# Performance work log

Measured on AMD Instinct MI355X. Metric: run time of the kernel, lower is better.

The kernel has to match this reference:

```python
import jax, jax.numpy as jnp
import numpy as np

NUM_HEADS = 12

def _get_rel_pos(size, rel_pos):
    # q_size == k_size == size, no interpolation needed (table has 2*size-1 rows)
    idx = jnp.arange(size)[:, None] - jnp.arange(size)[None, :] + (size - 1)  # (size,size)
    return rel_pos[idx]  # (size, size, head_dim)

def setup_inputs() -> dict:
    key = jax.random.key(0)
    ks = jax.random.split(key, 7)
    B, H, W, dim = 8, 32, 32, 768
    head_dim = dim // NUM_HEADS
    return {
        "x": jax.random.normal(ks[0], (B, H, W, dim), jnp.float32),
        "qkv_w": jax.random.normal(ks[1], (dim, 3 * dim), jnp.float32) * 0.02,
        "qkv_b": jax.random.normal(ks[2], (3 * dim,), jnp.float32) * 0.02,
        "proj_w": jax.random.normal(ks[3], (dim, dim), jnp.float32) * 0.02,
        "proj_b": jax.random.normal(ks[4], (dim,), jnp.float32) * 0.02,
        "rel_pos_h": jax.random.normal(ks[5], (2 * H - 1, head_dim), jnp.float32) * 0.02,
        "rel_pos_w": jax.random.normal(ks[6], (2 * W - 1, head_dim), jnp.float32) * 0.02,
    }

def reference(x, qkv_w, qkv_b, proj_w, proj_b, rel_pos_h, rel_pos_w):
    B, H, W, dim = x.shape
    N = H * W
    head_dim = dim // NUM_HEADS
    scale = head_dim ** (-0.5)

    qkv = x.reshape(B, N, dim) @ qkv_w + qkv_b                     # (B,N,3*dim)
    qkv = qkv.reshape(B, N, 3, NUM_HEADS, head_dim)
    qkv = qkv.transpose(2, 0, 3, 1, 4).reshape(3, B * NUM_HEADS, N, head_dim)
    q, k, v = qkv[0], qkv[1], qkv[2]                               # (B*h, N, hd)

    attn = jnp.einsum("bnd,bmd->bnm", q * scale, k)                # (B*h, N, N)

    # decomposed relative position bias
    Rh = _get_rel_pos(H, rel_pos_h)                                # (H,H,hd)
    Rw = _get_rel_pos(W, rel_pos_w)                                # (W,W,hd)
    r_q = q.reshape(B * NUM_HEADS, H, W, head_dim)
    rel_h = jnp.einsum("bhwc,hkc->bhwk", r_q, Rh)                  # (B*h,H,W,H)
    rel_w = jnp.einsum("bhwc,wkc->bhwk", r_q, Rw)                  # (B*h,H,W,W)
    attn = (attn.reshape(B * NUM_HEADS, H, W, H, W)
            + rel_h[:, :, :, :, None]
            + rel_w[:, :, :, None, :]).reshape(B * NUM_HEADS, N, N)

    attn = jax.nn.softmax(attn, axis=-1)
    out = jnp.einsum("bnm,bmd->bnd", attn, v)                      # (B*h, N, hd)
    out = out.reshape(B, NUM_HEADS, H, W, head_dim).transpose(0, 2, 3, 1, 4).reshape(B, H, W, dim)
    return out @ proj_w + proj_b
```

## Files before the change

### kernel.cpp

```cpp
#include <hip/hip_runtime.h>
#include <hip/hip_bf16.h>
#include <math.h>

#define DIM   768
#define NHEAD 12
#define NQ    1024

typedef short  short8  __attribute__((ext_vector_type(8)));
typedef unsigned short us8 __attribute__((ext_vector_type(8)));
typedef float  f32x16  __attribute__((ext_vector_type(16)));

#if __has_builtin(__builtin_amdgcn_exp2f)
#define EXP2(x) __builtin_amdgcn_exp2f(x)
#else
#define EXP2(x) __expf(0.69314718056f * (x))
#endif
#define LOG2E 1.44269504089f

__device__ inline ushort f2b(float f) {
  union { float f; unsigned u; } c; c.f = f;
  unsigned r = (c.u + 0x7FFFu + ((c.u >> 16) & 1u)) >> 16;
  return (ushort)r;
}
__device__ inline float b2f(ushort h) {
  union { unsigned u; float f; } c; c.u = ((unsigned)h) << 16;
  return c.f;
}
__device__ inline ushort4 cvt4(float4 v) {
  ushort4 o; o.x = f2b(v.x); o.y = f2b(v.y); o.z = f2b(v.z); o.w = f2b(v.w);
  return o;
}
__device__ inline unsigned pkr(float a, float b) {
  union { float f; unsigned u; } ca, cb; ca.f = a; cb.f = b;
  return __builtin_amdgcn_perm(cb.u + 0x8000u, ca.u + 0x8000u, 0x07060302u);
}
__device__ __forceinline__ void gload16(const void* g, void* l) {
  __builtin_amdgcn_global_load_lds(
      (const __attribute__((address_space(1))) void*)g,
      (__attribute__((address_space(3))) void*)l, 16, 0, 0);
}

__global__ __launch_bounds__(256) void prep(
    const float* __restrict__ x, const float* __restrict__ qkv_w,
    const float* __restrict__ proj_w, ushort* __restrict__ Xb,
    ushort* __restrict__ Wqt, ushort* __restrict__ Wpt) {
  __shared__ ushort Ts[64][68];
  const int blk = blockIdx.x, tid = threadIdx.x;
  if (blk < 768) {
    const float4* src = (const float4*)x;
    ushort4* dst = (ushort4*)Xb;
    int base = blk * 2048;
#pragma unroll
    for (int it = 0; it < 8; ++it) {
      int i = base + it * 256 + tid;
      dst[i] = cvt4(src[i]);
    }
    return;
  }
  const float* W; ushort* Wt; int ncols, tk, tn;
  if (blk < 1200) { int t = blk - 768;  W = qkv_w; Wt = Wqt; ncols = 2304; tk = t % 12; tn = t / 12; }
  else            { int t = blk - 1200; W = proj_w; Wt = Wpt; ncols = 768; tk = t % 12; tn = t / 12; }
  const int kb = tk * 64, nb = tn * 64;
#pragma unroll
  for (int rr = 0; rr < 4; ++rr) {
    int r = (tid >> 4) + rr * 16, c4 = (tid & 15) * 4;
    float4 w = *(const float4*)(W + (size_t)(kb + r) * ncols + nb + c4);
    *(ushort4*)&Ts[r][c4] = cvt4(w);
  }
  __syncthreads();
#pragma unroll
  for (int wwi = 0; wwi < 2; ++wwi) {
    int n = (tid >> 3) + wwi * 32, k8 = (tid & 7) * 8;
    us8 v;
#pragma unroll
    for (int j = 0; j < 8; ++j) v[j] = Ts[k8 + j][n];
    *(us8*)(Wt + (size_t)(nb + n) * 768 + kb + k8) = v;
  }
}

__global__ __launch_bounds__(256, 4) void gemm_qkv(
    const ushort* __restrict__ A, const ushort* __restrict__ BT,
    const float* __restrict__ bias, ushort* __restrict__ Cp,
    ushort* __restrict__ VTg) {
  __shared__ __align__(16) ushort As[128 * 64];
  __shared__ __align__(16) ushort Bs[128 * 64];
  const int tid = threadIdx.x;
  const int flat = blockIdx.x;
  const int g = flat >> 3;
  const int by = (flat & 7) * 8 + g / 18;
  const int bx = g % 18;
  const int bm = by * 128, bn = bx * 128;
  const int lane = tid & 63, wv = tid >> 6;
  const int l31 = lane & 31, lh = lane >> 5;
  const int wm = (wv >> 1) * 64, wn = (wv & 1) * 64;
  const int xr = l31 & 7;

  const int dr = lane >> 3;
  const int ccol = ((lane & 7) ^ dr) * 8;
  const ushort* ag = A + (size_t)(bm + wv * 32 + dr) * 768 + ccol;
  const ushort* bg = BT + (size_t)(bn + wv * 32 + dr) * 768 + ccol;
  ushort* al = &As[wv * 32 * 64];
  ushort* bl = &Bs[wv * 32 * 64];

  f32x16 acc[2][2];
#pragma unroll
  for (int i = 0; i < 2; ++i)
#pragma unroll
    for (int j = 0; j < 2; ++j)
#pragma unroll
      for (int r = 0; r < 16; ++r) acc[i][j][r] = 0.f;

  for (int kt = 0; kt < 768; kt += 64) {
    __syncthreads();
#pragma unroll
    for (int wi = 0; wi < 4; ++wi) {
      gload16(ag + kt + wi * (8 * 768), al + wi * 512);
      gload16(bg + kt + wi * (8 * 768), bl + wi * 512);
    }
    __syncthreads();
#pragma unroll
    for (int ks = 0; ks < 4; ++ks) {
      const int ca = ((ks * 2 + lh) ^ xr) * 8;
      short8 a0 = *(const short8*)&As[(wm + l31) * 64 + ca];
      short8 a1 = *(const short8*)&As[(wm + 32 + l31) * 64 + ca];
      short8 b0 = *(const short8*)&Bs[(wn + l31) * 64 + ca];
      short8 b1 = *(const short8*)&Bs[(wn + 32 + l31) * 64 + ca];
      acc[0][0] = __builtin_amdgcn_mfma_f32_32x32x16_bf16(a0, b0, acc[0][0], 0, 0, 0);
      acc[0][1] = __builtin_amdgcn_mfma_f32_32x32x16_bf16(a0, b1, acc[0][1], 0, 0, 0);
      acc[1][0] = __builtin_amdgcn_mfma_f32_32x32x16_bf16(a1, b0, acc[1][0], 0, 0, 0);
      acc[1][1] = __builtin_amdgcn_mfma_f32_32x32x16_bf16(a1, b1, acc[1][1], 0, 0, 0);
    }
  }

  if (bn < 1536) {
#pragma unroll
    for (int mb = 0; mb < 2; ++mb)
#pragma unroll
      for (int nb = 0; nb < 2; ++nb) {
        int col = bn + wn + nb * 32 + l31;
        float bv = bias[col];
#pragma unroll
        for (int reg = 0; reg < 16; ++reg) {
          int row = bm + wm + mb * 32 + (reg & 3) + 8 * (reg >> 2) + 4 * lh;
          Cp[(size_t)row * 2304 + col] = f2b(acc[mb][nb][reg] + bv);
        }
      }
  } else {
    const int b_ = bm >> 10;
    const int nbase = (bm & 1023) + wm;
#pragma unroll
    for (int nb = 0; nb < 2; ++nb) {
      int col = bn + wn + nb * 32 + l31;
      float bv = bias[col];
      int hd_ = col - 1536;
      int h_ = hd_ >> 6, d_ = hd_ & 63;
      ushort* vrow = VTg + ((size_t)(b_ * NHEAD + h_) * 64 + d_) * NQ;
#pragma unroll
      for (int mb = 0; mb < 2; ++mb)
#pragma unroll
        for (int g2 = 0; g2 < 4; ++g2) {
          int n = nbase + mb * 32 + 8 * g2 + 4 * lh;
          ushort4 st;
          st.x = f2b(acc[mb][nb][4 * g2 + 0] + bv);
          st.y = f2b(acc[mb][nb][4 * g2 + 1] + bv);
          st.z = f2b(acc[mb][nb][4 * g2 + 2] + bv);
          st.w = f2b(acc[mb][nb][4 * g2 + 3] + bv);
          *(ushort4*)(vrow + n) = st;
        }
    }
  }
}

__global__ __launch_bounds__(256, 4) void gemm_proj(
    const ushort* __restrict__ A, const ushort* __restrict__ BT,
    const float* __restrict__ bias, float* __restrict__ C) {
  __shared__ __align__(16) ushort As[128 * 64];
  __shared__ __align__(16) ushort Bs[64 * 64];
  const int tid = threadIdx.x;
  const int flat = blockIdx.x;
  const int g = flat >> 3;
  const int by = (flat & 7) * 8 + g / 12;
  const int bx = g % 12;
  const int bm = by * 128, bn = bx * 64;
  const int lane = tid & 63, wv = tid >> 6;
  const int l31 = lane & 31, lh = lane >> 5;
  const int wm = (wv >> 1) * 64, wn = (wv & 1) * 32;
  const int xr = l31 & 7;

  const int dr = lane >> 3;
  const int ccol = ((lane & 7) ^ dr) * 8;
  const ushort* ag = A + (size_t)(bm + wv * 32 + dr) * 768 + ccol;
  const ushort* bg = BT + (size_t)(bn + wv * 16 + dr) * 768 + ccol;
  ushort* al = &As[wv * 32 * 64];
  ushort* bl = &Bs[wv * 16 * 64];

  f32x16 acc0, acc1;
#pragma unroll
  for (int r = 0; r < 16; ++r) { acc0[r] = 0.f; acc1[r] = 0.f; }

  for (int kt = 0; kt < 768; kt += 64) {
    __syncthreads();
#pragma unroll
    for (int wi = 0; wi < 4; ++wi)
      gload16(ag + kt + wi * (8 * 768), al + wi * 512);
    gload16(bg + kt,            bl);
    gload16(bg + kt + 8 * 768,  bl + 512);
    __syncthreads();
#pragma unroll
    for (int ks = 0; ks < 4; ++ks) {
      const int ca = ((ks * 2 + lh) ^ xr) * 8;
      short8 a0 = *(const short8*)&As[(wm + l31) * 64 + ca];
      short8 a1 = *(const short8*)&As[(wm + 32 + l31) * 64 + ca];
      short8 b0 = *(const short8*)&Bs[(wn + l31) * 64 + ca];
      acc0 = __builtin_amdgcn_mfma_f32_32x32x16_bf16(a0, b0, acc0, 0, 0, 0);
      acc1 = __builtin_amdgcn_mfma_f32_32x32x16_bf16(a1, b0, acc1, 0, 0, 0);
    }
  }

  const int col = bn + wn + l31;
  const float bv = bias[col];
#pragma unroll
  for (int reg = 0; reg < 16; ++reg) {
    int row = bm + wm + (reg & 3) + 8 * (reg >> 2) + 4 * lh;
    C[(size_t)row * 768 + col]        = acc0[reg] + bv;
    C[(size_t)(row + 32) * 768 + col] = acc1[reg] + bv;
  }
}

__global__ __launch_bounds__(256, 4) void attn_mfma(
    const ushort* __restrict__ QKV, const ushort* __restrict__ VTg,
    const float* __restrict__ rph, const float* __restrict__ rpw,
    ushort* __restrict__ O) {
  __shared__ __align__(16) ushort L[16384];
  ushort* const R0 = L;
  ushort* const R1 = L + 8192;

  const int tid = threadIdx.x;
  const int bh = blockIdx.x % 96;
  const int qt = blockIdx.x / 96;
  const int b = bh / NHEAD, h = bh % NHEAD;
  const int n0 = qt * 128;
  const int lane = tid & 63, wv = tid >> 6;
  const int l31 = lane & 31, lh = lane >> 5;
  const int wb = wv * 32;
  const int xr = l31 & 7;
  const int px = l31 & 3;

  const ushort* qb = QKV + (size_t)b * NQ * 2304 + h * 64;
  const ushort* kb = qb + DIM;
  const ushort* vtg = VTg + (size_t)bh * 64 * NQ;

  const int dr = lane >> 3;
  const int ccol = ((lane & 7) ^ dr) * 8;

  {
    const ushort* qg = qb + (size_t)(n0 + wv * 32 + dr) * 2304 + ccol;
    ushort* ql = R0 + wv * 32 * 64;
#pragma unroll
    for (int wi = 0; wi < 4; ++wi)
      gload16(qg + (size_t)wi * 8 * 2304, ql + wi * 512);
  }
#pragma unroll
  for (int it = 0; it < 4; ++it) {
    int item = tid + 256 * it;
    int r = item >> 4, c4 = (item & 15) * 4;
    int sw = r * 64 + (((c4 >> 3) ^ (r & 7)) << 3) + (c4 & 7);
    if (r < 63) {
      float4 vh = *(const float4*)(rph + r * 64 + c4);
      vh.x *= LOG2E; vh.y *= LOG2E; vh.z *= LOG2E; vh.w *= LOG2E;
      *(ushort4*)&R1[sw] = cvt4(vh);
      float4 vw = *(const float4*)(rpw + r * 64 + c4);
      vw.x *= LOG2E; vw.y *= LOG2E; vw.z *= LOG2E; vw.w *= LOG2E;
      *(ushort4*)&R1[4096 + sw] = cvt4(vw);
    } else {
      ushort4 z = {0, 0, 0, 0};
      *(ushort4*)&R1[sw] = z;
      *(ushort4*)&R1[4096 + sw] = z;
    }
  }
  __syncthreads();

  short8 aq[4];
#pragma unroll
  for (int ks = 0; ks < 4; ++ks)
    aq[ks] = *(const short8*)&R0[(wb + l31) * 64 + ((ks * 2 + lh) ^ xr) * 8];

  const int rA = qt * 4 + wv + 31 - l31;
  short8 ah[4];
#pragma unroll
  for (int ks = 0; ks < 4; ++ks)
    ah[ks] = *(const short8*)&R1[rA * 64 + ((ks * 2 + lh) ^ (rA & 7)) * 8];
  __syncthreads();

  ushort* Pb2 = R0 + wv * 1024;
  ushort* rhs = R0 + 4096;

  {
    f32x16 sh;
#pragma unroll
    for (int i = 0; i < 16; ++i) sh[i] = 0.f;
#pragma unroll
    for (int ks = 0; ks < 4; ++ks)
      sh = __builtin_amdgcn_mfma_f32_32x32x16_bf16(ah[ks], aq[ks], sh, 0, 0, 0);
#pragma unroll
    for (int reg = 0; reg < 16; ++reg) {
      int rm = (reg & 3) + 8 * (reg >> 2) + 4 * lh;
      rhs[rm * 128 + wb + l31] = f2b(sh[reg]);
    }
  }

  short8 aw[8];
#pragma unroll
  for (int ub = 0; ub < 2; ++ub) {
    const int rB = ub * 32 + l31;
#pragma unroll
    for (int ks = 0; ks < 4; ++ks)
      aw[ub * 4 + ks] =
          *(const short8*)&R1[4096 + rB * 64 + ((ks * 2 + lh) ^ (rB & 7)) * 8];
  }
  __syncthreads();

  float rwv[16];
  {
    f32x16 su0;
#pragma unroll
    for (int i = 0; i < 16; ++i) su0[i] = 0.f;
#pragma unroll
    for (int ks = 0; ks < 4; ++ks)
      su0 = __builtin_amdgcn_mfma_f32_32x32x16_bf16(aw[ks], aq[ks], su0, 0, 0, 0);
#pragma unroll
    for (int reg = 0; reg < 16; ++reg) {
      int rm = (reg & 3) + 8 * (reg >> 2) + 4 * lh;
      R1[rm * 128 + wb + l31] = f2b(su0[reg]);
    }
    f32x16 su1;
#pragma unroll
    for (int i = 0; i < 16; ++i) su1[i] = 0.f;
#pragma unroll
    for (int ks = 0; ks < 4; ++ks)
      su1 = __builtin_amdgcn_mfma_f32_32x32x16_bf16(aw[4 + ks], aq[ks], su1, 0, 0, 0);
#pragma unroll
    for (int reg = 0; reg < 16; ++reg) {
      int rm = (reg & 3) + 8 * (reg >> 2) + 4 * lh;
      R1[(32 + rm) * 128 + wb + l31] = f2b(su1[reg]);
    }
#pragma unroll
    for (int reg = 0; reg < 16; ++reg) {
      int rm = (reg & 3) + 8 * (reg >> 2) + 4 * lh;
      rwv[reg] = b2f(R1[(31 + l31 - rm) * 128 + wb + l31]);
    }
  }

  const ushort* kg = kb + (size_t)(wv * 16 + dr) * 2304 + ccol;
  const ushort* vg = vtg + (size_t)(wv * 16 + dr) * NQ + ccol;
  ushort* kl = R1 + wv * 16 * 64;
  ushort* vl = R1 + 4096 + wv * 16 * 64;

  f32x16 oacc0, oacc1;
#pragma unroll
  for (int i = 0; i < 16; ++i) { oacc0[i] = 0.f; oacc1[i] = 0.f; }
  float lacc = 0.f;

  for (int t = 0; t < 16; ++t) {
    const int kt = t * 64;
    __syncthreads();
    gload16(kg + (size_t)kt * 2304,              kl);
    gload16(kg + (size_t)kt * 2304 + 8 * 2304,   kl + 512);
    gload16(vg + kt,                             vl);
    gload16(vg + kt + 8 * NQ,                    vl + 512);
    __syncthreads();

    const float rh0 = b2f(rhs[(2 * t) * 128 + wb + l31]);
    const float rh1 = b2f(rhs[(2 * t + 1) * 128 + wb + l31]);

#pragma unroll
    for (int cb = 0; cb < 2; ++cb) {
      f32x16 s;
#pragma unroll
      for (int i = 0; i < 16; ++i) s[i] = 0.f;
#pragma unroll
      for (int ks = 0; ks < 4; ++ks) {
        const int ck = ((ks * 2 + lh) ^ xr) * 8;
        short8 ak = *(const short8*)&R1[(cb * 32 + l31) * 64 + ck];
        s = __builtin_amdgcn_mfma_f32_32x32x16_bf16(ak, aq[ks], s, 0, 0, 0);
      }
      const float rhv = cb ? rh1 : rh0;
#pragma unroll
      for (int g = 0; g < 4; ++g) {
        float p0 = EXP2(fmaf(s[4 * g + 0], 0.18033688f, rwv[4 * g + 0] + rhv));
        float p1 = EXP2(fmaf(s[4 * g + 1], 0.18033688f, rwv[4 * g + 1] + rhv));
        float p2 = EXP2(fmaf(s[4 * g + 2], 0.18033688f, rwv[4 * g + 2] + rhv));
        float p3 = EXP2(fmaf(s[4 * g + 3], 0.18033688f, rwv[4 * g + 3] + rhv));
        lacc += (p0 + p1) + (p2 + p3);
        uint2 pk; pk.x = pkr(p0, p1); pk.y = pkr(p2, p3);
        *(uint2*)&Pb2[l31 * 32 + ((g ^ px) * 8) + 4 * lh] = pk;
      }
#pragma unroll
      for (int ks = 0; ks < 2; ++ks) {
        const int cv = ((cb * 4 + ks * 2 + lh) ^ xr) * 8;
        short8 ap  = *(const short8*)&Pb2[l31 * 32 + ((ks * 2 + lh) ^ px) * 8];
        short8 bv0 = *(const short8*)&R1[4096 + l31 * 64 + cv];
        short8 bv1 = *(const short8*)&R1[4096 + (32 + l31) * 64 + cv];
        oacc0 = __builtin_amdgcn_mfma_f32_32x32x16_bf16(ap, bv0, oacc0, 0, 0, 0);
        oacc1 = __builtin_amdgcn_mfma_f32_32x32x16_bf16(ap, bv1, oacc1, 0, 0, 0);
      }
    }
  }

  lacc += __shfl_xor(lacc, 32);
  const float linv = 1.0f / lacc;
  ushort* ob = O + ((size_t)b * NQ + n0 + wb) * DIM + h * 64;
#pragma unroll
  for (int reg = 0; reg < 16; ++reg) {
    int row = (reg & 3) + 8 * (reg >> 2) + 4 * lh;
    float lq = __shfl(linv, row);
    ob[(size_t)row * DIM + l31]      = f2b(oacc0[reg] * lq);
    ob[(size_t)row * DIM + 32 + l31] = f2b(oacc1[reg] * lq);
  }
}

extern "C" void kernel_launch(void* const* d_in, const int* in_sizes, int n_in,
                              void* d_out, int out_size, void* d_ws, size_t ws_size,
                              hipStream_t stream) {
  const float* x      = (const float*)d_in[0];
  const float* qkv_w  = (const float*)d_in[1];
  const float* qkv_b  = (const float*)d_in[2];
  const float* proj_w = (const float*)d_in[3];
  const float* proj_b = (const float*)d_in[4];
  const float* rel_h  = (const float*)d_in[5];
  const float* rel_w  = (const float*)d_in[6];
  float* out = (float*)d_out;

  ushort* qkvb = (ushort*)d_ws;
  ushort* obuf = qkvb + (size_t)8192 * 2304;
  ushort* Xb   = obuf + (size_t)8192 * DIM;
  ushort* Wqt  = Xb + (size_t)8192 * DIM;
  ushort* Wpt  = Wqt + (size_t)2304 * DIM;
  ushort* VTg  = Wpt + (size_t)DIM * DIM;

  prep<<<dim3(1344), 256, 0, stream>>>(x, qkv_w, proj_w, Xb, Wqt, Wpt);

  gemm_qkv<<<dim3(1152), 256, 0, stream>>>(Xb, Wqt, qkv_b, qkvb, VTg);

  attn_mfma<<<dim3(96 * 8), 256, 0, stream>>>(qkvb, VTg, rel_h, rel_w, obuf);

  gemm_proj<<<dim3(768), 256, 0, stream>>>(obuf, Wpt, proj_b, out);
}
```

Baseline: 203.4 us.

## Double-buffer K/V tiles in attention kernel and pad P staging buffer

Splits the shared-memory tile region into two K/V buffers and prefetches the next 64-key tile while computing on the current one, dropping one barrier per iteration. The P staging buffer moves from an XOR swizzle to a padded row stride of 40. Rel-pos table loads are also hoisted and the two rel-w MFMA chains interleaved. This raises LDS use and lowers launch bounds occupancy from 4 to 3 blocks per CU, trading occupancy for overlap of global loads with MFMA work.

```diff
diff --git a/kernel.cpp b/kernel.cpp
--- a/kernel.cpp
+++ b/kernel.cpp
@@ -227,13 +227,13 @@
   }
 }
 
-__global__ __launch_bounds__(256, 4) void attn_mfma(
+__global__ __launch_bounds__(256, 3) void attn_mfma(
     const ushort* __restrict__ QKV, const ushort* __restrict__ VTg,
     const float* __restrict__ rph, const float* __restrict__ rpw,
     ushort* __restrict__ O) {
-  __shared__ __align__(16) ushort L[16384];
-  ushort* const R0 = L;
-  ushort* const R1 = L + 8192;
+  __shared__ __align__(16) ushort R0[9216];
+  __shared__ __align__(16) ushort B0[8192];
+  __shared__ __align__(16) ushort B1[8192];
 
   const int tid = threadIdx.x;
   const int bh = blockIdx.x % 96;
@@ -244,7 +244,6 @@
   const int l31 = lane & 31, lh = lane >> 5;
   const int wb = wv * 32;
   const int xr = l31 & 7;
-  const int px = l31 & 3;
 
   const ushort* qb = QKV + (size_t)b * NQ * 2304 + h * 64;
   const ushort* kb = qb + DIM;
@@ -268,14 +267,14 @@
     if (r < 63) {
       float4 vh = *(const float4*)(rph + r * 64 + c4);
       vh.x *= LOG2E; vh.y *= LOG2E; vh.z *= LOG2E; vh.w *= LOG2E;
-      *(ushort4*)&R1[sw] = cvt4(vh);
+      *(ushort4*)&B0[sw] = cvt4(vh);
       float4 vw = *(const float4*)(rpw + r * 64 + c4);
       vw.x *= LOG2E; vw.y *= LOG2E; vw.z *= LOG2E; vw.w *= LOG2E;
-      *(ushort4*)&R1[4096 + sw] = cvt4(vw);
+      *(ushort4*)&B1[sw] = cvt4(vw);
     } else {
       ushort4 z = {0, 0, 0, 0};
-      *(ushort4*)&R1[sw] = z;
-      *(ushort4*)&R1[4096 + sw] = z;
+      *(ushort4*)&B0[sw] = z;
+      *(ushort4*)&B1[sw] = z;
     }
   }
   __syncthreads();
@@ -289,11 +288,20 @@
   short8 ah[4];
 #pragma unroll
   for (int ks = 0; ks < 4; ++ks)
-    ah[ks] = *(const short8*)&R1[rA * 64 + ((ks * 2 + lh) ^ (rA & 7)) * 8];
+    ah[ks] = *(const short8*)&B0[rA * 64 + ((ks * 2 + lh) ^ (rA & 7)) * 8];
+  short8 aw[8];
+#pragma unroll
+  for (int ub = 0; ub < 2; ++ub) {
+    const int rB = ub * 32 + l31;
+#pragma unroll
+    for (int ks = 0; ks < 4; ++ks)
+      aw[ub * 4 + ks] =
+          *(const short8*)&B1[rB * 64 + ((ks * 2 + lh) ^ (rB & 7)) * 8];
+  }
   __syncthreads();
 
-  ushort* Pb2 = R0 + wv * 1024;
-  ushort* rhs = R0 + 4096;
+  ushort* Pb2 = R0 + wv * 1280;
+  ushort* rhs = R0 + 5120;
 
   {
     f32x16 sh;
@@ -308,53 +316,38 @@
       rhs[rm * 128 + wb + l31] = f2b(sh[reg]);
     }
   }
-
-  short8 aw[8];
-#pragma unroll
-  for (int ub = 0; ub < 2; ++ub) {
-    const int rB = ub * 32 + l31;
-#pragma unroll
-    for (int ks = 0; ks < 4; ++ks)
-      aw[ub * 4 + ks] =
-          *(const short8*)&R1[4096 + rB * 64 + ((ks * 2 + lh) ^ (rB & 7)) * 8];
-  }
-  __syncthreads();
-
   float rwv[16];
   {
-    f32x16 su0;
-#pragma unroll
-    for (int i = 0; i < 16; ++i) su0[i] = 0.f;
-#pragma unroll
-    for (int ks = 0; ks < 4; ++ks)
-      su0 = __builtin_amdgcn_mfma_f32_32x32x16_bf16(aw[ks], aq[ks], su0, 0, 0, 0);
+    f32x16 su0, su1;
+#pragma unroll
+    for (int i = 0; i < 16; ++i) { su0[i] = 0.f; su1[i] = 0.f; }
+#pragma unroll
+    for (int ks = 0; ks < 4; ++ks) {
+      su0 = __builtin_amdgcn_mfma_f32_32x32x16_bf16(aw[ks],     aq[ks], su0, 0, 0, 0);
+      su1 = __builtin_amdgcn_mfma_f32_32x32x16_bf16(aw[4 + ks], aq[ks], su1, 0, 0, 0);
+    }
 #pragma unroll
     for (int reg = 0; reg < 16; ++reg) {
       int rm = (reg & 3) + 8 * (reg >> 2) + 4 * lh;
-      R1[rm * 128 + wb + l31] = f2b(su0[reg]);
-    }
-    f32x16 su1;
-#pragma unroll
-    for (int i = 0; i < 16; ++i) su1[i] = 0.f;
-#pragma unroll
-    for (int ks = 0; ks < 4; ++ks)
-      su1 = __builtin_amdgcn_mfma_f32_32x32x16_bf16(aw[4 + ks], aq[ks], su1, 0, 0, 0);
+      B0[rm * 128 + wb + l31]        = f2b(su0[reg]);
+      B0[(32 + rm) * 128 + wb + l31] = f2b(su1[reg]);
+    }
 #pragma unroll
     for (int reg = 0; reg < 16; ++reg) {
       int rm = (reg & 3) + 8 * (reg >> 2) + 4 * lh;
-      R1[(32 + rm) * 128 + wb + l31] = f2b(su1[reg]);
-    }
-#pragma unroll
-    for (int reg = 0; reg < 16; ++reg) {
-      int rm = (reg & 3) + 8 * (reg >> 2) + 4 * lh;
-      rwv[reg] = b2f(R1[(31 + l31 - rm) * 128 + wb + l31]);
-    }
-  }
+      rwv[reg] = b2f(B0[(31 + l31 - rm) * 128 + wb + l31]);
+    }
+  }
+  __syncthreads();
 
   const ushort* kg = kb + (size_t)(wv * 16 + dr) * 2304 + ccol;
   const ushort* vg = vtg + (size_t)(wv * 16 + dr) * NQ + ccol;
-  ushort* kl = R1 + wv * 16 * 64;
-  ushort* vl = R1 + 4096 + wv * 16 * 64;
+  const int so = wv * 1024;
+
+  gload16(kg,            B0 + so);
+  gload16(kg + 8 * 2304, B0 + so + 512);
+  gload16(vg,            B0 + 4096 + so);
+  gload16(vg + 8 * NQ,   B0 + 4096 + so + 512);
 
   f32x16 oacc0, oacc1;
 #pragma unroll
@@ -362,13 +355,16 @@
   float lacc = 0.f;
 
   for (int t = 0; t < 16; ++t) {
-    const int kt = t * 64;
     __syncthreads();
-    gload16(kg + (size_t)kt * 2304,              kl);
-    gload16(kg + (size_t)kt * 2304 + 8 * 2304,   kl + 512);
-    gload16(vg + kt,                             vl);
-    gload16(vg + kt + 8 * NQ,                    vl + 512);
-    __syncthreads();
+    ushort* Bt = (t & 1) ? B1 : B0;
+    if (t < 15) {
+      ushort* Bn = (t & 1) ? B0 : B1;
+      const size_t kn = (size_t)(t + 1) * 64;
+      gload16(kg + kn * 2304,            Bn + so);
+      gload16(kg + kn * 2304 + 8 * 2304, Bn + so + 512);
+      gload16(vg + kn,                   Bn + 4096 + so);
+      gload16(vg + kn + 8 * NQ,          Bn + 4096 + so + 512);
+    }
 
     const float rh0 = b2f(rhs[(2 * t) * 128 + wb + l31]);
     const float rh1 = b2f(rhs[(2 * t + 1) * 128 + wb + l31]);
@@ -381,7 +377,7 @@
 #pragma unroll
       for (int ks = 0; ks < 4; ++ks) {
         const int ck = ((ks * 2 + lh) ^ xr) * 8;
-        short8 ak = *(const short8*)&R1[(cb * 32 + l31) * 64 + ck];
+        short8 ak = *(const short8*)&Bt[(cb * 32 + l31) * 64 + ck];
         s = __builtin_amdgcn_mfma_f32_32x32x16_bf16(ak, aq[ks], s, 0, 0, 0);
       }
       const float rhv = cb ? rh1 : rh0;
@@ -393,14 +389,14 @@
         float p3 = EXP2(fmaf(s[4 * g + 3], 0.18033688f, rwv[4 * g + 3] + rhv));
         lacc += (p0 + p1) + (p2 + p3);
         uint2 pk; pk.x = pkr(p0, p1); pk.y = pkr(p2, p3);
-        *(uint2*)&Pb2[l31 * 32 + ((g ^ px) * 8) + 4 * lh] = pk;
+        *(uint2*)&Pb2[l31 * 40 + 8 * g + 4 * lh] = pk;
       }
 #pragma unroll
       for (int ks = 0; ks < 2; ++ks) {
         const int cv = ((cb * 4 + ks * 2 + lh) ^ xr) * 8;
-        short8 ap  = *(const short8*)&Pb2[l31 * 32 + ((ks * 2 + lh) ^ px) * 8];
-        short8 bv0 = *(const short8*)&R1[4096 + l31 * 64 + cv];
-        short8 bv1 = *(const short8*)&R1[4096 + (32 + l31) * 64 + cv];
+        short8 ap  = *(const short8*)&Pb2[l31 * 40 + ks * 16 + lh * 8];
+        short8 bv0 = *(const short8*)&Bt[4096 + l31 * 64 + cv];
+        short8 bv1 = *(const short8*)&Bt[4096 + (32 + l31) * 64 + cv];
         oacc0 = __builtin_amdgcn_mfma_f32_32x32x16_bf16(ap, bv0, oacc0, 0, 0, 0);
         oacc1 = __builtin_amdgcn_mfma_f32_32x32x16_bf16(ap, bv1, oacc1, 0, 0, 0);
       }
```

After: 193.8 us. -4.7%, faster.
